# Optimization experiments

Measured on AMD Instinct MI355X. Metric: run time of the kernel, lower is better.

Reference implementation:

```python
import jax, jax.numpy as jnp
import numpy as np

N, E, H, R = 20000, 320000, 64, 32
CUTOFF = 5.0
EYE3 = jnp.eye(3, dtype=jnp.float32)


def _decompose(X):
    # X: [..., 3, 3] -> (I trace part, A antisymmetric, S traceless symmetric)
    tr = jnp.trace(X, axis1=-2, axis2=-1)
    I = tr[..., None, None] / 3.0 * EYE3
    A = (X - jnp.swapaxes(X, -1, -2)) / 2.0
    S = (X + jnp.swapaxes(X, -1, -2)) / 2.0 - I
    return I, A, S


def _tnorm(X):
    return (X ** 2).sum((-2, -1))


def _mix(T, W):
    # channel-wise Linear without bias: Linear applied after permute(0,2,3,1)
    return jnp.einsum('nhij,gh->ngij', T, W)


def setup_inputs() -> dict:
    key = jax.random.key(0)
    ks = jax.random.split(key, 8)
    s = 0.05
    X = jax.random.normal(ks[0], (N, H, 3, 3), jnp.float32)
    edge_index = jax.random.randint(ks[1], (2, E), 0, N, dtype=jnp.int64)
    edge_dist = jax.random.uniform(ks[2], (E,), jnp.float32) * CUTOFF
    edge_attr = jax.random.normal(ks[3], (E, R), jnp.float32)
    w1 = jax.random.normal(ks[4], (H, R), jnp.float32) * s
    b1 = jnp.zeros((H,), jnp.float32)
    w2 = jax.random.normal(ks[5], (2 * H, H), jnp.float32) * s
    b2 = jnp.zeros((2 * H,), jnp.float32)
    w3 = jax.random.normal(ks[6], (3 * H, 2 * H), jnp.float32) * s
    b3 = jnp.zeros((3 * H,), jnp.float32)
    lin_w = jax.random.normal(ks[7], (6, H, H), jnp.float32) * s
    return dict(X=X, edge_index=edge_index, edge_dist=edge_dist, edge_attr=edge_attr,
                w1=w1, b1=b1, w2=w2, b2=b2, w3=w3, b3=b3, lin_w=lin_w)


def reference(X, edge_index, edge_dist, edge_attr, w1, b1, w2, b2, w3, b3, lin_w):
    row, col = edge_index[0], edge_index[1]
    # CosineCutoff: 0.5*(cos(pi*d/cutoff)+1) inside cutoff
    C = 0.5 * (jnp.cos(edge_dist * (jnp.pi / CUTOFF)) + 1.0) * (edge_dist < CUTOFF).astype(edge_dist.dtype)
    h = jax.nn.silu(edge_attr @ w1.T + b1)
    h = jax.nn.silu(h @ w2.T + b2)
    edge_feat = ((h @ w3.T + b3) * C[:, None]).reshape(E, H, 3)
    Xn = X / (_tnorm(X) + 1.0)[..., None, None]
    I, A, S = _decompose(Xn)
    I = _mix(I, lin_w[0])
    A = _mix(A, lin_w[1])
    S = _mix(S, lin_w[2])
    Y = I + A + S

    def msg(f, T):  # gather tensor[col], weight by edge factor, scatter-add to row
        return jax.ops.segment_sum(f[:, :, None, None] * T[col], row, num_segments=N)

    M = msg(edge_feat[..., 0], I) + msg(edge_feat[..., 1], A) + msg(edge_feat[..., 2], S)
    prod = jnp.matmul(M, Y) + jnp.matmul(Y, M)  # O(3) branch
    I2, A2, S2 = _decompose(prod)
    norm = (_tnorm(I2 + A2 + S2) + 1.0)[..., None, None]
    dX = _mix(I2 / norm, lin_w[3]) + _mix(A2 / norm, lin_w[4]) + _mix(S2 / norm, lin_w[5])
    return Xn + dX + jnp.matmul(dX, dX)
```

## Files before the change

kernel.cpp:

```cpp
#include <hip/hip_runtime.h>
#include <hip/hip_fp16.h>
#include <hip/hip_bf16.h>

#define NR 32

typedef __attribute__((ext_vector_type(8))) short bf8_t;
typedef __attribute__((ext_vector_type(4))) float f4_t;

__device__ __forceinline__ float silu_f(float x) {
    return x * __builtin_amdgcn_rcpf(1.0f + __expf(-x));
}

__device__ __forceinline__ unsigned pkbf(float lo, float hi) {
    __hip_bfloat162 h = __float22bfloat162_rn(make_float2(lo, hi));
    union { __hip_bfloat162 h2; unsigned u; } cv; cv.h2 = h; return cv.u;
}
__device__ __forceinline__ float bf_lo(unsigned u) { return __uint_as_float(u << 16); }
__device__ __forceinline__ float bf_hi(unsigned u) { return __uint_as_float(u & 0xffff0000u); }

__device__ __forceinline__ float rdl(float v, int l) {
    return __int_as_float(__builtin_amdgcn_readlane(__float_as_int(v), l));
}

__global__ __launch_bounds__(256) void k_hist(
    const int* __restrict__ eidx, int* __restrict__ cnt, int nedges)
{
    int e = blockIdx.x * 256 + threadIdx.x;
    if (e < nedges) atomicAdd(&cnt[eidx[e]], 1);
}

__global__ __launch_bounds__(1024) void k_scan2(
    int* __restrict__ cnt, int* __restrict__ off, int n)
{
    __shared__ int wsum[16];
    __shared__ int wbase[16];
    const int tid = threadIdx.x;
    const int lane = tid & 63, wid = tid >> 6;
    const int per = (n + 1023) >> 10;
    const int base = tid * per;
    int s = 0;
    for (int i = 0; i < per; i++) {
        int idx = base + i;
        if (idx < n) s += cnt[idx];
    }
    int incl = s;
    for (int d = 1; d < 64; d <<= 1) {
        int t = __shfl_up(incl, d);
        if (lane >= d) incl += t;
    }
    if (lane == 63) wsum[wid] = incl;
    __syncthreads();
    if (wid == 0) {
        int v = (lane < 16) ? wsum[lane] : 0;
        int inc2 = v;
        for (int d = 1; d < 16; d <<= 1) {
            int t = __shfl_up(inc2, d);
            if (lane >= d) inc2 += t;
        }
        if (lane < 16) wbase[lane] = inc2 - v;
        if (lane == 15) off[n] = inc2;
    }
    __syncthreads();
    int run = wbase[wid] + incl - s;
    for (int i = 0; i < per; i++) {
        int idx = base + i;
        if (idx < n) {
            int v = cnt[idx];
            off[idx] = run;
            cnt[idx] = run;
            run += v;
        }
    }
}

__global__ __launch_bounds__(256) void k_scatter(
    const int* __restrict__ eidx, int* __restrict__ cur,
    int* __restrict__ perm, int* __restrict__ col_s, int nedges)
{
    int e = blockIdx.x * 256 + threadIdx.x;
    if (e < nedges) {
        int r = eidx[e];
        int pos = atomicAdd(&cur[r], 1);
        perm[pos] = e;
        col_s[pos] = eidx[nedges + e];
    }
}

__global__ __launch_bounds__(256) void k_prep(
    const float* __restrict__ w1, const float* __restrict__ b1,
    const float* __restrict__ w2, const float* __restrict__ b2,
    const float* __restrict__ w3, const float* __restrict__ b3,
    unsigned* __restrict__ wpre)
{
    int i = blockIdx.x * 256 + threadIdx.x;
    if (i < 12288) {
        int mk = i >> 8, m = mk >> 2, kt = mk & 3;
        int rr = (i >> 4) & 15, gg = (i >> 2) & 3, dd = i & 3;
        int row = 16 * m + rr;
        int c0 = 32 * kt + 16 * (dd >> 1) + 4 * gg + 2 * (dd & 1);
        const float* s = w3 + (size_t)row * 128 + c0;
        wpre[i] = pkbf(s[0], s[1]);
    } else if (i < 12672) {
        int j = i - 12288;
        float v = (j < 64) ? b1[j] : (j < 192) ? b2[j - 64] : b3[j - 192];
        wpre[i] = __float_as_uint(v);
    } else if (i < 13696) {
        int j = i - 12672;
        int m = j >> 8, rr = (j >> 4) & 15, gg = (j >> 2) & 3, dd = j & 3;
        const float* s = w1 + (size_t)(16 * m + rr) * 32 + 8 * gg + 2 * dd;
        wpre[i] = pkbf(s[0], s[1]);
    } else if (i < 17792) {
        int j = i - 13696;
        int mk = j >> 8, m = mk >> 1, kt = mk & 1;
        int rr = (j >> 4) & 15, gg = (j >> 2) & 3, dd = j & 3;
        int row = 16 * m + rr;
        int c0 = 32 * kt + 16 * (dd >> 1) + 4 * gg + 2 * (dd & 1);
        const float* s = w2 + (size_t)row * 64 + c0;
        wpre[i] = pkbf(s[0], s[1]);
    }
}

__global__ __launch_bounds__(512) void k1_node_mix(
    const float* __restrict__ X, const float* __restrict__ lw,
    unsigned* __restrict__ Tmh, int nnodes)
{
    __shared__ float Wl[3 * 64 * 68];
    const int tid = threadIdx.x;
#pragma unroll
    for (int k = 0; k < 6; k++) {
        int l = (tid + k * 512) * 4;
        int row = l >> 6, col = l & 63;
        *(float4*)&Wl[row * 68 + col] = *(const float4*)(lw + l);
    }

    const int wid = tid >> 6, lane = tid & 63;
    const int n = blockIdx.x * 8 + wid;
    const bool valid = (n < nnodes);

    float i0 = 0, i1 = 0, i2 = 0, i3 = 0, i4 = 0, i5 = 0, i6 = 0, i7 = 0, i8 = 0;
    if (valid) {
        const float* xp = X + ((size_t)n * 64 + lane) * 9;
        float v[9];
#pragma unroll
        for (int i = 0; i < 9; i++) v[i] = xp[i];
        float tn = 0.f;
#pragma unroll
        for (int i = 0; i < 9; i++) tn = fmaf(v[i], v[i], tn);
        float inv = 1.0f / (tn + 1.0f);
#pragma unroll
        for (int i = 0; i < 9; i++) v[i] *= inv;
        float lam = (v[0] + v[4] + v[8]) * (1.0f / 3.0f);
        i0 = lam;
        i1 = (v[1] - v[3]) * 0.5f;
        i2 = (v[2] - v[6]) * 0.5f;
        i3 = (v[5] - v[7]) * 0.5f;
        i4 = v[0] - lam;
        i5 = (v[1] + v[3]) * 0.5f;
        i6 = (v[2] + v[6]) * 0.5f;
        i7 = v[4] - lam;
        i8 = (v[5] + v[7]) * 0.5f;
    }
    __syncthreads();

    const int g = lane;
    float a0 = 0, a1 = 0, a2 = 0, a3 = 0, a4 = 0, a5 = 0, a6 = 0, a7 = 0, a8 = 0;
#pragma unroll
    for (int h4 = 0; h4 < 64; h4 += 4) {
        float4 w0 = *(const float4*)&Wl[g * 68 + h4];
        float4 w1 = *(const float4*)&Wl[(64 + g) * 68 + h4];
        float4 w2 = *(const float4*)&Wl[(128 + g) * 68 + h4];
#pragma unroll
        for (int j = 0; j < 4; j++) {
            const int h = h4 + j;
            float wa = (&w0.x)[j], wb = (&w1.x)[j], wc = (&w2.x)[j];
            a0 = fmaf(wa, rdl(i0, h), a0);
            a1 = fmaf(wb, rdl(i1, h), a1);
            a2 = fmaf(wb, rdl(i2, h), a2);
            a3 = fmaf(wb, rdl(i3, h), a3);
            a4 = fmaf(wc, rdl(i4, h), a4);
            a5 = fmaf(wc, rdl(i5, h), a5);
            a6 = fmaf(wc, rdl(i6, h), a6);
            a7 = fmaf(wc, rdl(i7, h), a7);
            a8 = fmaf(wc, rdl(i8, h), a8);
        }
    }
    if (valid) {
        unsigned* outp = Tmh + (size_t)n * 320 + g;
        outp[0 * 64] = pkbf(a0, a1);
        outp[1 * 64] = pkbf(a2, a3);
        outp[2 * 64] = pkbf(a4, a5);
        outp[3 * 64] = pkbf(a6, a7);
        outp[4 * 64] = pkbf(a8, 0.f);
    }
}

#define LBI 49152
#define LEF 50688
#define EFS 408
#define NW  16

__global__ __launch_bounds__(1024, 4) void k2f_fused(
    const float* __restrict__ ea, const float* __restrict__ dist,
    const int* __restrict__ perm, const int* __restrict__ col_s,
    const int* __restrict__ off, const unsigned* __restrict__ wpre,
    const unsigned* __restrict__ Tmh, float* __restrict__ out, int nrows)
{
    __shared__ __align__(16) char smem[LEF + NW * 16 * EFS];
    const int tid = threadIdx.x;

#pragma unroll
    for (int k = 0; k < 4; k++) {
        int idx = tid + k * 1024;
        if (idx < 3168)
            ((uint4*)smem)[idx] = ((const uint4*)wpre)[idx];
    }

    const int wid = tid >> 6, lane = tid & 63;
    const int r16 = lane & 15, g = lane >> 4;
    const int slot = r16 * 4 + g;
    char* efb = smem + LEF + wid * (16 * EFS);

    bf8_t aw1[4];
#pragma unroll
    for (int m = 0; m < 4; m++)
        aw1[m] = *(const bf8_t*)(wpre + 12672 + (m * 64 + slot) * 4);
    bf8_t aw2[8][2];
#pragma unroll
    for (int m = 0; m < 8; m++)
#pragma unroll
        for (int kt = 0; kt < 2; kt++)
            aw2[m][kt] = *(const bf8_t*)(wpre + 13696 + ((m * 2 + kt) * 64 + slot) * 4);
    __syncthreads();

    const int r = blockIdx.x * NW + wid;
    if (r >= nrows) return;
    const int beg = off[r];
    const int deg = off[r + 1] - beg;

    float acc[9];
#pragma unroll
    for (int i = 0; i < 9; i++) acc[i] = 0.f;

    float4 nv0 = {0, 0, 0, 0}, nv1 = {0, 0, 0, 0};
    float nd = 1e9f;
    int nval = 0;
    if (deg > 0) {
        int cnt0 = min(16, deg);
        int e0 = perm[beg + ((r16 < cnt0) ? r16 : 0)];
        const float* ar0 = ea + (size_t)e0 * NR + 8 * g;
        nv0 = *(const float4*)(ar0);
        nv1 = *(const float4*)(ar0 + 4);
        nd = dist[e0];
        nval = (r16 < cnt0) ? 1 : 0;
    }

#pragma unroll 1
    for (int c0 = 0; c0 < deg; c0 += 16) {
        const int cnt = min(16, deg - c0);

        bf8_t bx;
        {
            union { bf8_t v; unsigned u[4]; } tt;
            tt.u[0] = pkbf(nv0.x, nv0.y); tt.u[1] = pkbf(nv0.z, nv0.w);
            tt.u[2] = pkbf(nv1.x, nv1.y); tt.u[3] = pkbf(nv1.z, nv1.w);
            bx = tt.v;
        }
        float cf = (nval && nd < 5.0f)
                 ? 0.5f * (__cosf(nd * 0.62831853071795864f) + 1.0f) : 0.0f;

        unsigned pk1[4][2];
#pragma unroll
        for (int m = 0; m < 4; m++) {
            f4_t c = *(const f4_t*)(smem + LBI + (16 * m + 4 * g) * 4);
            c = __builtin_amdgcn_mfma_f32_16x16x32_bf16(aw1[m], bx, c, 0, 0, 0);
            pk1[m][0] = pkbf(silu_f(c[0]), silu_f(c[1]));
            pk1[m][1] = pkbf(silu_f(c[2]), silu_f(c[3]));
        }
        bf8_t B2[2];
        {
            union { bf8_t v; unsigned u[4]; } ta, tb;
            ta.u[0] = pk1[0][0]; ta.u[1] = pk1[0][1]; ta.u[2] = pk1[1][0]; ta.u[3] = pk1[1][1];
            tb.u[0] = pk1[2][0]; tb.u[1] = pk1[2][1]; tb.u[2] = pk1[3][0]; tb.u[3] = pk1[3][1];
            B2[0] = ta.v; B2[1] = tb.v;
        }

        unsigned pk2[8][2];
#pragma unroll
        for (int m = 0; m < 8; m++) {
            f4_t c = *(const f4_t*)(smem + LBI + (64 + 16 * m + 4 * g) * 4);
            c = __builtin_amdgcn_mfma_f32_16x16x32_bf16(aw2[m][0], B2[0], c, 0, 0, 0);
            c = __builtin_amdgcn_mfma_f32_16x16x32_bf16(aw2[m][1], B2[1], c, 0, 0, 0);
            pk2[m][0] = pkbf(silu_f(c[0]), silu_f(c[1]));
            pk2[m][1] = pkbf(silu_f(c[2]), silu_f(c[3]));
        }
        bf8_t B3[4];
#pragma unroll
        for (int kt = 0; kt < 4; kt++) {
            union { bf8_t v; unsigned u[4]; } tt;
            tt.u[0] = pk2[2 * kt][0]; tt.u[1] = pk2[2 * kt][1];
            tt.u[2] = pk2[2 * kt + 1][0]; tt.u[3] = pk2[2 * kt + 1][1];
            B3[kt] = tt.v;
        }

        {
            int c1 = c0 + 16;
            if (c1 < deg) {
                int cnt1 = min(16, deg - c1);
                int e1 = perm[beg + c1 + ((r16 < cnt1) ? r16 : 0)];
                const float* ar1 = ea + (size_t)e1 * NR + 8 * g;
                nv0 = *(const float4*)(ar1);
                nv1 = *(const float4*)(ar1 + 4);
                nd = dist[e1];
                nval = (r16 < cnt1) ? 1 : 0;
            }
        }

        asm volatile("s_waitcnt lgkmcnt(0)" ::: "memory");
        __builtin_amdgcn_sched_barrier(0);

#pragma unroll
        for (int m = 0; m < 12; m++) {
            f4_t c = *(const f4_t*)(smem + LBI + (192 + 16 * m + 4 * g) * 4);
#pragma unroll
            for (int kt = 0; kt < 4; kt++) {
                bf8_t aw = *(const bf8_t*)(smem + ((m * 4 + kt) * 64 + slot) * 16);
                c = __builtin_amdgcn_mfma_f32_16x16x32_bf16(aw, B3[kt], c, 0, 0, 0);
            }
            union { struct { __half2 a, b; } h; uint2 u; } pu;
            pu.h.a = __float22half2_rn(make_float2(c[0] * cf, c[1] * cf));
            pu.h.b = __float22half2_rn(make_float2(c[2] * cf, c[3] * cf));
            *(uint2*)(efb + r16 * EFS + (16 * m + 4 * g) * 2) = pu.u;
        }
        asm volatile("s_waitcnt lgkmcnt(0)" ::: "memory");
        __builtin_amdgcn_sched_barrier(0);

#pragma unroll 4
        for (int s = 0; s < cnt; s++) {
            int col = col_s[beg + c0 + s];
            const unsigned* t = Tmh + (size_t)col * 320 + lane;
            unsigned q0 = t[0], q1 = t[64], q2 = t[128], q3 = t[192], q4 = t[256];
            const __half* fp = (const __half*)(efb + s * EFS + 6 * lane);
            float f0 = __half2float(fp[0]);
            float f1 = __half2float(fp[1]);
            float f2 = __half2float(fp[2]);
            acc[0] = fmaf(f0, bf_lo(q0), acc[0]);
            acc[1] = fmaf(f1, bf_hi(q0), acc[1]);
            acc[2] = fmaf(f1, bf_lo(q1), acc[2]);
            acc[3] = fmaf(f1, bf_hi(q1), acc[3]);
            acc[4] = fmaf(f2, bf_lo(q2), acc[4]);
            acc[5] = fmaf(f2, bf_hi(q2), acc[5]);
            acc[6] = fmaf(f2, bf_lo(q3), acc[6]);
            acc[7] = fmaf(f2, bf_hi(q3), acc[7]);
            acc[8] = fmaf(f2, bf_lo(q4), acc[8]);
        }
    }

    float y[9];
    {
        const unsigned* tp = Tmh + (size_t)r * 320 + lane;
        unsigned q0 = tp[0], q1 = tp[64], q2 = tp[128], q3 = tp[192], q4 = tp[256];
        y[0] = bf_lo(q0); y[1] = bf_hi(q0); y[2] = bf_lo(q1); y[3] = bf_hi(q1);
        y[4] = bf_lo(q2); y[5] = bf_hi(q2); y[6] = bf_lo(q3); y[7] = bf_hi(q3);
        y[8] = bf_lo(q4);
    }
    float Y[9], Mm[9];
    Y[0] = y[0] + y[4]; Y[1] = y[1] + y[5]; Y[2] = y[2] + y[6];
    Y[3] = -y[1] + y[5]; Y[4] = y[0] + y[7]; Y[5] = y[3] + y[8];
    Y[6] = -y[2] + y[6]; Y[7] = -y[3] + y[8]; Y[8] = y[0] - y[4] - y[7];
    Mm[0] = acc[0] + acc[4]; Mm[1] = acc[1] + acc[5]; Mm[2] = acc[2] + acc[6];
    Mm[3] = -acc[1] + acc[5]; Mm[4] = acc[0] + acc[7]; Mm[5] = acc[3] + acc[8];
    Mm[6] = -acc[2] + acc[6]; Mm[7] = -acc[3] + acc[8]; Mm[8] = acc[0] - acc[4] - acc[7];
    float P[9];
#pragma unroll
    for (int a = 0; a < 3; a++)
#pragma unroll
        for (int b = 0; b < 3; b++) {
            float s = 0.f;
#pragma unroll
            for (int c = 0; c < 3; c++) {
                s = fmaf(Mm[a * 3 + c], Y[c * 3 + b], s);
                s = fmaf(Y[a * 3 + c], Mm[c * 3 + b], s);
            }
            P[a * 3 + b] = s;
        }
    float tn = 0.f;
#pragma unroll
    for (int k = 0; k < 9; k++) tn = fmaf(P[k], P[k], tn);
    float inv = 1.0f / (tn + 1.0f);
    float lam = (P[0] + P[4] + P[8]) * (1.0f / 3.0f);

    float* mp = out + (size_t)r * 576 + lane;
    mp[0 * 64] = lam * inv;
    mp[1 * 64] = (P[1] - P[3]) * 0.5f * inv;
    mp[2 * 64] = (P[2] - P[6]) * 0.5f * inv;
    mp[3 * 64] = (P[5] - P[7]) * 0.5f * inv;
    mp[4 * 64] = (P[0] - lam) * inv;
    mp[5 * 64] = (P[1] + P[3]) * 0.5f * inv;
    mp[6 * 64] = (P[2] + P[6]) * 0.5f * inv;
    mp[7 * 64] = (P[4] - lam) * inv;
    mp[8 * 64] = (P[5] + P[7]) * 0.5f * inv;
}

__global__ __launch_bounds__(512) void k4_final(
    const float* __restrict__ X, const float* __restrict__ lw,
    float* __restrict__ out, int nnodes)
{
    __shared__ float Wl[3 * 64 * 68];
    const int tid = threadIdx.x;
#pragma unroll
    for (int k = 0; k < 6; k++) {
        int l = (tid + k * 512) * 4;
        int row = l >> 6, col = l & 63;
        *(float4*)&Wl[row * 68 + col] = *(const float4*)(lw + 3 * 4096 + l);
    }

    const int wid = tid >> 6, lane = tid & 63;
    const int n = blockIdx.x * 8 + wid;
    const bool valid = (n < nnodes);

    float i0 = 0, i1 = 0, i2 = 0, i3 = 0, i4 = 0, i5 = 0, i6 = 0, i7 = 0, i8 = 0;
    if (valid) {
        const float* pp = out + (size_t)n * 576 + lane;
        i0 = pp[0 * 64]; i1 = pp[1 * 64]; i2 = pp[2 * 64];
        i3 = pp[3 * 64]; i4 = pp[4 * 64]; i5 = pp[5 * 64];
        i6 = pp[6 * 64]; i7 = pp[7 * 64]; i8 = pp[8 * 64];
    }
    __syncthreads();

    const int g = lane;
    float a0 = 0, a1 = 0, a2 = 0, a3 = 0, a4 = 0, a5 = 0, a6 = 0, a7 = 0, a8 = 0;
#pragma unroll
    for (int h4 = 0; h4 < 64; h4 += 4) {
        float4 w0 = *(const float4*)&Wl[g * 68 + h4];
        float4 w1 = *(const float4*)&Wl[(64 + g) * 68 + h4];
        float4 w2 = *(const float4*)&Wl[(128 + g) * 68 + h4];
#pragma unroll
        for (int j = 0; j < 4; j++) {
            const int h = h4 + j;
            float wa = (&w0.x)[j], wb = (&w1.x)[j], wc = (&w2.x)[j];
            a0 = fmaf(wa, rdl(i0, h), a0);
            a1 = fmaf(wb, rdl(i1, h), a1);
            a2 = fmaf(wb, rdl(i2, h), a2);
            a3 = fmaf(wb, rdl(i3, h), a3);
            a4 = fmaf(wc, rdl(i4, h), a4);
            a5 = fmaf(wc, rdl(i5, h), a5);
            a6 = fmaf(wc, rdl(i6, h), a6);
            a7 = fmaf(wc, rdl(i7, h), a7);
            a8 = fmaf(wc, rdl(i8, h), a8);
        }
    }

    if (valid) {
        float D[9];
        D[0] = a0 + a4; D[1] = a1 + a5; D[2] = a2 + a6;
        D[3] = -a1 + a5; D[4] = a0 + a7; D[5] = a3 + a8;
        D[6] = -a2 + a6; D[7] = -a3 + a8; D[8] = a0 - a4 - a7;

        const float* xp = X + ((size_t)n * 64 + g) * 9;
        float xv[9];
#pragma unroll
        for (int i = 0; i < 9; i++) xv[i] = xp[i];
        float tn = 0.f;
#pragma unroll
        for (int i = 0; i < 9; i++) tn = fmaf(xv[i], xv[i], tn);
        float inv = 1.0f / (tn + 1.0f);

        float* op = out + ((size_t)n * 64 + g) * 9;
        float res[9];
#pragma unroll
        for (int a = 0; a < 3; a++)
#pragma unroll
            for (int b = 0; b < 3; b++) {
                float dd = 0.f;
#pragma unroll
                for (int c = 0; c < 3; c++) dd = fmaf(D[a * 3 + c], D[c * 3 + b], dd);
                res[a * 3 + b] = xv[a * 3 + b] * inv + D[a * 3 + b] + dd;
            }
#pragma unroll
        for (int i = 0; i < 9; i++) op[i] = res[i];
    }
}

extern "C" void kernel_launch(void* const* d_in, const int* in_sizes, int n_in,
                              void* d_out, int out_size, void* d_ws, size_t ws_size,
                              hipStream_t stream)
{
    const float* X    = (const float*)d_in[0];
    const int*   eidx = (const int*)d_in[1];
    const float* dist = (const float*)d_in[2];
    const float* ea   = (const float*)d_in[3];
    const float* w1   = (const float*)d_in[4];
    const float* b1   = (const float*)d_in[5];
    const float* w2   = (const float*)d_in[6];
    const float* b2   = (const float*)d_in[7];
    const float* w3   = (const float*)d_in[8];
    const float* b3   = (const float*)d_in[9];
    const float* lw   = (const float*)d_in[10];
    float* outp = (float*)d_out;

    const int nnodes = in_sizes[0] / (64 * 9);
    const int nedges = in_sizes[2];

    unsigned* Tmh  = (unsigned*)d_ws;
    int* cur       = (int*)(Tmh + (size_t)nnodes * 320);
    int* off       = cur + nnodes;
    int* perm      = off + nnodes + 1;
    int* col_s     = perm + nedges;
    unsigned* wpre = (unsigned*)(col_s + nedges);

    hipMemsetAsync(cur, 0, (size_t)nnodes * sizeof(int), stream);
    k_hist<<<(nedges + 255) / 256, 256, 0, stream>>>(eidx, cur, nedges);
    k_scan2<<<1, 1024, 0, stream>>>(cur, off, nnodes);
    k_scatter<<<(nedges + 255) / 256, 256, 0, stream>>>(eidx, cur, perm, col_s, nedges);
    k_prep<<<70, 256, 0, stream>>>(w1, b1, w2, b2, w3, b3, wpre);

    k1_node_mix<<<(nnodes + 7) / 8, 512, 0, stream>>>(X, lw, Tmh, nnodes);
    k2f_fused<<<(nnodes + NW - 1) / NW, 1024, 0, stream>>>(ea, dist, perm, col_s, off, wpre, Tmh, outp, nnodes);
    k4_final<<<(nnodes + 7) / 8, 512, 0, stream>>>(X, lw, outp, nnodes);
}
```

Measured before the change: 430.9 us.

## Prefetch gathered neighbor tensors before edge-MLP MFMA to hide gather latency

The scatter loop used to load each neighbor's packed tensor row serially after the third MLP layer. Now each lane loads one column index per 16-edge chunk and broadcasts it with readlane. The first 12 neighbor rows are issued as loads before the layer-3 MFMAs, and the last 4 are loaded mid-accumulation into reused registers, so global gather latency overlaps matrix work. The accumulation loop is fully unrolled over 16 slots. Padded slots clamp to a valid column and contribute zero, because their cutoff factor is zero. The cost is about 60 extra live VGPRs and redundant loads for partial chunks, which may lower occupancy.

```diff
diff --git a/kernel.cpp b/kernel.cpp
--- a/kernel.cpp
+++ b/kernel.cpp
@@ -258,6 +258,8 @@
     for (int c0 = 0; c0 < deg; c0 += 16) {
         const int cnt = min(16, deg - c0);
 
+        int colv = col_s[beg + c0 + ((r16 < cnt) ? r16 : (cnt - 1))];
+
         bf8_t bx;
         {
             union { bf8_t v; unsigned u[4]; } tt;
@@ -300,6 +302,15 @@
             tt.u[0] = pk2[2 * kt][0]; tt.u[1] = pk2[2 * kt][1];
             tt.u[2] = pk2[2 * kt + 1][0]; tt.u[3] = pk2[2 * kt + 1][1];
             B3[kt] = tt.v;
+        }
+
+        unsigned q[12][5];
+#pragma unroll
+        for (int s = 0; s < 12; s++) {
+            int sc = __builtin_amdgcn_readlane(colv, s);
+            const unsigned* t = Tmh + (size_t)(unsigned)sc * 320 + lane;
+            q[s][0] = t[0]; q[s][1] = t[64]; q[s][2] = t[128];
+            q[s][3] = t[192]; q[s][4] = t[256];
         }
 
         {
@@ -334,25 +345,35 @@
         asm volatile("s_waitcnt lgkmcnt(0)" ::: "memory");
         __builtin_amdgcn_sched_barrier(0);
 
-#pragma unroll 4
-        for (int s = 0; s < cnt; s++) {
-            int col = col_s[beg + c0 + s];
-            const unsigned* t = Tmh + (size_t)col * 320 + lane;
-            unsigned q0 = t[0], q1 = t[64], q2 = t[128], q3 = t[192], q4 = t[256];
-            const __half* fp = (const __half*)(efb + s * EFS + 6 * lane);
-            float f0 = __half2float(fp[0]);
-            float f1 = __half2float(fp[1]);
-            float f2 = __half2float(fp[2]);
-            acc[0] = fmaf(f0, bf_lo(q0), acc[0]);
-            acc[1] = fmaf(f1, bf_hi(q0), acc[1]);
-            acc[2] = fmaf(f1, bf_lo(q1), acc[2]);
-            acc[3] = fmaf(f1, bf_hi(q1), acc[3]);
-            acc[4] = fmaf(f2, bf_lo(q2), acc[4]);
-            acc[5] = fmaf(f2, bf_hi(q2), acc[5]);
-            acc[6] = fmaf(f2, bf_lo(q3), acc[6]);
-            acc[7] = fmaf(f2, bf_hi(q3), acc[7]);
-            acc[8] = fmaf(f2, bf_lo(q4), acc[8]);
-        }
+#define ACC_STEP(S, Q)                                                        \
+        {                                                                     \
+            const __half* fp = (const __half*)(efb + (S) * EFS + 6 * lane);   \
+            float f0 = __half2float(fp[0]);                                   \
+            float f1 = __half2float(fp[1]);                                   \
+            float f2 = __half2float(fp[2]);                                   \
+            acc[0] = fmaf(f0, bf_lo(Q[0]), acc[0]);                           \
+            acc[1] = fmaf(f1, bf_hi(Q[0]), acc[1]);                           \
+            acc[2] = fmaf(f1, bf_lo(Q[1]), acc[2]);                           \
+            acc[3] = fmaf(f1, bf_hi(Q[1]), acc[3]);                           \
+            acc[4] = fmaf(f2, bf_lo(Q[2]), acc[4]);                           \
+            acc[5] = fmaf(f2, bf_hi(Q[2]), acc[5]);                           \
+            acc[6] = fmaf(f2, bf_lo(Q[3]), acc[6]);                           \
+            acc[7] = fmaf(f2, bf_hi(Q[3]), acc[7]);                           \
+            acc[8] = fmaf(f2, bf_lo(Q[4]), acc[8]);                           \
+        }
+
+        ACC_STEP(0, q[0]) ACC_STEP(1, q[1]) ACC_STEP(2, q[2]) ACC_STEP(3, q[3])
+#pragma unroll
+        for (int s = 12; s < 16; s++) {
+            int sc = __builtin_amdgcn_readlane(colv, s);
+            const unsigned* t = Tmh + (size_t)(unsigned)sc * 320 + lane;
+            q[s - 12][0] = t[0]; q[s - 12][1] = t[64]; q[s - 12][2] = t[128];
+            q[s - 12][3] = t[192]; q[s - 12][4] = t[256];
+        }
+        ACC_STEP(4, q[4])  ACC_STEP(5, q[5])  ACC_STEP(6, q[6])  ACC_STEP(7, q[7])
+        ACC_STEP(8, q[8])  ACC_STEP(9, q[9])  ACC_STEP(10, q[10]) ACC_STEP(11, q[11])
+        ACC_STEP(12, q[0]) ACC_STEP(13, q[1]) ACC_STEP(14, q[2])  ACC_STEP(15, q[3])
+#undef ACC_STEP
     }
 
     float y[9];
```

New measurement: 573.6 us. 1.33x slower.
